# Kernel tuning notes

Measured on AMD Instinct MI355X. Metric: run time of the kernel, lower is better.

Reference implementation:

```python
import jax, jax.numpy as jnp
import numpy as np

B, L, D, O = 4, 2048, 4096, 4096   # batch, seq, in_features, out_features
P = 2                               # n_pack
NF = 2000                           # n_frequency
NFP = NF // P                       # frequencies per pack
IN_P, OUT_P = D // P, O // P        # per-pack spectrum grid
NGATE = P * D // 10                 # gate parameter count
SCALING = 150.0


def setup_inputs() -> dict:
    key = jax.random.key(0)
    ks = jax.random.split(key, 6)
    x = jax.random.normal(ks[0], (B, L, D), dtype=jnp.float32)
    base_w = jax.random.normal(ks[1], (O, D), dtype=jnp.float32) * 0.02
    base_b = jax.random.normal(ks[2], (O,), dtype=jnp.float32) * 0.02
    spectrum = jax.random.normal(ks[3], (P, NFP), dtype=jnp.float32)
    B_list = jax.random.normal(ks[4], (P, P, P), dtype=jnp.float32) * 0.5
    gate_param = jax.random.normal(ks[5], (NGATE,), dtype=jnp.float32)
    # unique random frequency locations per pack (mirrors torch.randperm)
    rng = np.random.default_rng(777)
    idx = jnp.asarray(np.stack([rng.permutation(OUT_P * IN_P)[:NFP] for _ in range(P)]), dtype=jnp.int64)
    gidx = jnp.asarray(rng.permutation(P * D)[:NGATE], dtype=jnp.int64)
    return {"x": x, "base_w": base_w, "base_b": base_b, "spectrum": spectrum,
            "B_list": B_list, "gate_param": gate_param, "idx": idx, "gidx": gidx}


def _delta_weight(spec_i, idx_i, B_i, dtype):
    # scatter sparse spectrum into (OUT_P, IN_P) grid
    dense = jnp.zeros((OUT_P, IN_P), dtype).at[idx_i // IN_P, idx_i % IN_P].set(spec_i)
    A = jnp.fft.ifft2(dense).real  # (OUT_P, IN_P)
    # kron(A, B_i) -> (O, D)
    return SCALING * (A[:, None, :, None] * B_i[None, :, None, :]).reshape(O, D)


def reference(x, base_w, base_b, spectrum, B_list, gate_param, idx, gidx):
    dt = x.dtype
    # base linear
    result = jnp.einsum('bld,od->blo', x, base_w) + base_b
    # gate matrix: scatter then ifft2
    gate_m = jnp.zeros((P, D), dt).at[gidx // D, gidx % D].set(gate_param)
    gate_m = jnp.fft.ifft2(gate_m).real  # (P, D)
    gate_w = jax.nn.softmax(jnp.einsum('bld,ed->ble', x, gate_m), axis=-1)  # (B,L,P)
    # per-pack delta weights and outputs
    deltas = jax.vmap(lambda s, i, b: _delta_weight(s, i, b, dt))(spectrum, idx, B_list)  # (P,O,D)
    outputs = jnp.einsum('bld,pod->blpo', x, deltas)  # (B,L,P,O)
    final = jnp.einsum('blpo,blp->blo', outputs, gate_w)
    return (result + final).astype(dt)
```

## Files before the change

### kernel.cpp

```cpp
#include <hip/hip_runtime.h>


#define AS1 __attribute__((address_space(1)))
#define AS3 __attribute__((address_space(3)))

using bf16x8   = __attribute__((ext_vector_type(8))) __bf16;
using f32x4    = __attribute__((ext_vector_type(4))) float;
using ushort8v = __attribute__((ext_vector_type(8))) unsigned short;
using ushort4v = __attribute__((ext_vector_type(4))) unsigned short;

__device__ __forceinline__ unsigned short f2bf(float f) {
  unsigned int u = __float_as_uint(f);
  u += 0x7FFFu + ((u >> 16) & 1u);
  return (unsigned short)(u >> 16);
}

__device__ __forceinline__ void gll16(void* lds, const void* g) {
  __builtin_amdgcn_global_load_lds((AS1 void*)(g), (AS3 void*)(lds), 16, 0, 0);
}

__global__ void k_gatem(const float* __restrict__ gp, const int* __restrict__ gidx,
                        float* __restrict__ gatem, int NG) {
  int t = blockIdx.x * 256 + threadIdx.x;
  int e = t >> 12, d = t & 4095;
  float acc = 0.f;
  for (int k = 0; k < NG; k++) {
    int iv = gidx[k];
    int dk = iv & 4095;
    float th = (float)((d * dk) & 4095) * 1.5339807878856412e-3f;
    float cv = __cosf(th);
    float v = gp[k] * cv;
    acc += ((e & (iv >> 12)) & 1) ? -v : v;
  }
  gatem[t] = acc * (1.f / 8192.f);
}

__global__ void k_tables(const float* __restrict__ spec, const int* __restrict__ idx,
                         unsigned short* __restrict__ tbl, int NFP) {
  int z = blockIdx.y;
  int p = z >> 1, isQ = z & 1;
  int t = blockIdx.x * 256 + threadIdx.x;
  int r = t >> 11, kk = t & 2047;
  unsigned short v = 0;
  if (kk < 2 * NFP) {
    int j = (kk < NFP) ? kk : kk - NFP;
    int iv = idx[p * NFP + j];
    int f = isQ ? (iv & 2047) : (iv >> 11);
    float th = (float)((r * f) & 2047) * 3.0679615757712823e-3f;
    float val = (kk < NFP) ? __cosf(th) : __sinf(th);
    if (isQ) {
      float s = spec[p * NFP + j];
      val *= (kk < NFP) ? s : -s;
    }
    v = f2bf(val);
  }
  tbl[(size_t)z * 4194304 + t] = v;
}

__global__ void k_gate(const float* __restrict__ x, const float* __restrict__ gatem,
                       float* __restrict__ g) {
  int n = blockIdx.x * 4 + (threadIdx.x >> 6);
  int l = threadIdx.x & 63;
  const float4* xr  = (const float4*)(x + (size_t)n * 4096);
  const float4* g0p = (const float4*)(gatem);
  const float4* g1p = (const float4*)(gatem + 4096);
  float s0 = 0.f, s1 = 0.f;
  for (int t = 0; t < 16; t++) {
    int ii = l + (t << 6);
    float4 xv = xr[ii], a = g0p[ii], b = g1p[ii];
    s0 += xv.x * a.x + xv.y * a.y + xv.z * a.z + xv.w * a.w;
    s1 += xv.x * b.x + xv.y * b.y + xv.z * b.z + xv.w * b.w;
  }
  for (int off = 32; off > 0; off >>= 1) {
    s0 += __shfl_down(s0, off);
    s1 += __shfl_down(s1, off);
  }
  if (l == 0) {
    float mx = fmaxf(s0, s1);
    float e0 = __expf(s0 - mx), e1 = __expf(s1 - mx);
    float inv = 1.f / (e0 + e1);
    g[2 * n] = e0 * inv;
    g[2 * n + 1] = e1 * inv;
  }
}

__global__ void k_convx(const float* __restrict__ x, unsigned short* __restrict__ xb,
                        unsigned short* __restrict__ Zg, const float* __restrict__ Bl,
                        const float* __restrict__ g) {
  size_t t = (size_t)blockIdx.x * 256 + threadIdx.x;
  const float4* xp = (const float4*)x + t * 2;
  float4 v0 = xp[0], v1 = xp[1];
  ushort8v xv;
  xv[0]=f2bf(v0.x); xv[1]=f2bf(v0.y); xv[2]=f2bf(v0.z); xv[3]=f2bf(v0.w);
  xv[4]=f2bf(v1.x); xv[5]=f2bf(v1.y); xv[6]=f2bf(v1.z); xv[7]=f2bf(v1.w);
  *(ushort8v*)(xb + t * 8) = xv;
  int n = (int)(t >> 9);
  int c0 = ((int)t & 511) * 4;
  float gg[2] = {g[2 * n], g[2 * n + 1]};
  float xe[4] = {v0.x, v0.z, v1.x, v1.z};
  float xo[4] = {v0.y, v0.w, v1.y, v1.w};
  #pragma unroll
  for (int pa = 0; pa < 4; pa++) {
    int p = pa >> 1, a = pa & 1;
    float b0 = Bl[pa * 2] * gg[p], b1 = Bl[pa * 2 + 1] * gg[p];
    ushort4v yv;
    #pragma unroll
    for (int c = 0; c < 4; c++) yv[c] = f2bf(b0 * xe[c] + b1 * xo[c]);
    *(ushort4v*)(Zg + (size_t)a * 33554432 + (size_t)n * 4096 + p * 2048 + c0) = yv;
  }
}

__global__ void k_convw(const float* __restrict__ w, unsigned short* __restrict__ wb) {
  size_t t = (size_t)blockIdx.x * 256 + threadIdx.x;
  const float4* sp = (const float4*)w + t * 2;
  float4 v0 = sp[0], v1 = sp[1];
  ushort8v o;
  o[0]=f2bf(v0.x); o[1]=f2bf(v0.y); o[2]=f2bf(v0.z); o[3]=f2bf(v0.w);
  o[4]=f2bf(v1.x); o[5]=f2bf(v1.y); o[6]=f2bf(v1.z); o[7]=f2bf(v1.w);
  *(ushort8v*)(wb + t * 8) = o;
}

__device__ __forceinline__ void gemm_core(
    const unsigned short* __restrict__ Amat, int lda,
    const unsigned short* __restrict__ Bmat, int ldb,
    int K, char* As, char* Bs, f32x4 acc[4][4]) {
  const int tid = threadIdx.x;
  const int w = tid >> 6, l = tid & 63;
  const int quad = l >> 4, l15 = l & 15;
  const int wm = (w >> 1) << 6, wn = (w & 1) << 6;

  int c1 = (w << 6) + l, c2 = c1 + 256;
  int r1 = c1 >> 2, q1 = (c1 & 3) ^ ((r1 >> 1) & 3);
  int r2 = c2 >> 2, q2 = (c2 & 3) ^ ((r2 >> 1) & 3);
  const unsigned short* aS1 = Amat + (size_t)r1 * lda + (q1 << 3);
  const unsigned short* aS2 = Amat + (size_t)r2 * lda + (q2 << 3);
  const unsigned short* bS1 = Bmat + (size_t)r1 * ldb + (q1 << 3);
  const unsigned short* bS2 = Bmat + (size_t)r2 * ldb + (q2 << 3);
  char* aD1 = As + (w << 10);
  char* aD2 = As + 4096 + (w << 10);
  char* bD1 = Bs + (w << 10);
  char* bD2 = Bs + 4096 + (w << 10);

  int aOff[4], bOff[4];
  #pragma unroll
  for (int i = 0; i < 4; i++) {
    int ra = wm + (i << 4) + l15;
    aOff[i] = (ra << 6) + ((quad ^ ((ra >> 1) & 3)) << 4);
    int rb = wn + (i << 4) + l15;
    bOff[i] = (rb << 6) + ((quad ^ ((rb >> 1) & 3)) << 4);
  }

  for (int kt = 0; kt < K; kt += 32) {
    __syncthreads();
    gll16(aD1, aS1); gll16(aD2, aS2);
    gll16(bD1, bS1); gll16(bD2, bS2);
    __syncthreads();
    bf16x8 af[4], bfv[4];
    #pragma unroll
    for (int i = 0; i < 4; i++) af[i]  = *(const bf16x8*)(As + aOff[i]);
    #pragma unroll
    for (int j = 0; j < 4; j++) bfv[j] = *(const bf16x8*)(Bs + bOff[j]);
    #pragma unroll
    for (int i = 0; i < 4; i++)
      #pragma unroll
      for (int j = 0; j < 4; j++)
        acc[i][j] = __builtin_amdgcn_mfma_f32_16x16x32_bf16(af[i], bfv[j], acc[i][j], 0, 0, 0);
    aS1 += 32; aS2 += 32; bS1 += 32; bS2 += 32;
  }
}

__global__ __launch_bounds__(256, 2) void k_abuild(
    const unsigned short* __restrict__ tbl, unsigned short* __restrict__ Acat) {
  __shared__ __align__(16) char sm[16384];
  const int p = blockIdx.z;
  const unsigned short* P = tbl + (size_t)(2 * p) * 4194304;
  const unsigned short* Q = tbl + (size_t)(2 * p + 1) * 4194304;
  f32x4 acc[4][4];
  #pragma unroll
  for (int i = 0; i < 4; i++)
    #pragma unroll
    for (int j = 0; j < 4; j++) acc[i][j] = (f32x4){0.f, 0.f, 0.f, 0.f};
  const int m0 = blockIdx.x << 7, n0 = blockIdx.y << 7;
  gemm_core(P + (size_t)m0 * 2048, 2048, Q + (size_t)n0 * 2048, 2048, 2048,
            sm, sm + 8192, acc);
  const int tid = threadIdx.x, w = tid >> 6, l = tid & 63;
  const int quad = l >> 4, l15 = l & 15;
  const int wm = (w >> 1) << 6, wn = (w & 1) << 6;
  const float SC = 150.f / 4194304.f;
  unsigned short* Ap = Acat + (size_t)p * 2048;
  #pragma unroll
  for (int j = 0; j < 4; j++) {
    int c = n0 + wn + (j << 4) + l15;
    #pragma unroll
    for (int i = 0; i < 4; i++) {
      int rb = m0 + wm + (i << 4) + (quad << 2);
      #pragma unroll
      for (int reg = 0; reg < 4; reg++)
        Ap[(size_t)(rb + reg) * 4096 + c] = f2bf(acc[i][j][reg] * SC);
    }
  }
}

__global__ __launch_bounds__(256, 2) void k_base(
    const unsigned short* __restrict__ xb, const unsigned short* __restrict__ wb,
    const float* __restrict__ bias, float* __restrict__ out) {
  __shared__ __align__(16) char sm[16384];
  f32x4 acc[4][4];
  #pragma unroll
  for (int i = 0; i < 4; i++)
    #pragma unroll
    for (int j = 0; j < 4; j++) acc[i][j] = (f32x4){0.f, 0.f, 0.f, 0.f};
  const int m0 = blockIdx.y << 7, n0 = blockIdx.x << 7;
  gemm_core(xb + (size_t)m0 * 4096, 4096, wb + (size_t)n0 * 4096, 4096, 4096,
            sm, sm + 8192, acc);
  const int tid = threadIdx.x, w = tid >> 6, l = tid & 63;
  const int quad = l >> 4, l15 = l & 15;
  const int wm = (w >> 1) << 6, wn = (w & 1) << 6;
  #pragma unroll
  for (int j = 0; j < 4; j++) {
    int o = n0 + wn + (j << 4) + l15;
    float bv = bias[o];
    #pragma unroll
    for (int i = 0; i < 4; i++) {
      int mb = m0 + wm + (i << 4) + (quad << 2);
      #pragma unroll
      for (int reg = 0; reg < 4; reg++)
        out[(size_t)(mb + reg) * 4096 + o] = acc[i][j][reg] + bv;
    }
  }
}

__global__ __launch_bounds__(256, 2) void k_pack(
    const unsigned short* __restrict__ Zg, const unsigned short* __restrict__ Acat,
    float* __restrict__ out) {
  __shared__ __align__(16) char sm[16384];
  char* Z0s = sm; char* Z1s = sm + 4096; char* Bs = sm + 8192;
  const int tid = threadIdx.x, w = tid >> 6, l = tid & 63;
  const int quad = l >> 4, l15 = l & 15;
  const int m0 = blockIdx.y << 6, r0 = blockIdx.x << 7;
  const int wm = (w >> 1) << 5, wn = (w & 1) << 6;

  int c1 = (w << 6) + l, c2 = c1 + 256;
  int rz = c1 >> 2, qz = (c1 & 3) ^ ((rz >> 1) & 3);
  int rb1 = c1 >> 2, qb1 = qz;
  int rb2 = c2 >> 2, qb2 = (c2 & 3) ^ ((rb2 >> 1) & 3);

  const unsigned short* z0S = Zg + (size_t)(m0 + rz) * 4096 + (qz << 3);
  const unsigned short* z1S = z0S + 33554432;
  const unsigned short* bS1 = Acat + (size_t)(r0 + rb1) * 4096 + (qb1 << 3);
  const unsigned short* bS2 = Acat + (size_t)(r0 + rb2) * 4096 + (qb2 << 3);
  char* z0D = Z0s + (w << 10);
  char* z1D = Z1s + (w << 10);
  char* bD1 = Bs + (w << 10);
  char* bD2 = Bs + 4096 + (w << 10);

  int zOff[2], bOff[4];
  #pragma unroll
  for (int i = 0; i < 2; i++) {
    int ra = wm + (i << 4) + l15;
    zOff[i] = (ra << 6) + ((quad ^ ((ra >> 1) & 3)) << 4);
  }
  #pragma unroll
  for (int j = 0; j < 4; j++) {
    int rb = wn + (j << 4) + l15;
    bOff[j] = (rb << 6) + ((quad ^ ((rb >> 1) & 3)) << 4);
  }

  f32x4 acc[2][2][4];
  #pragma unroll
  for (int a = 0; a < 2; a++)
    #pragma unroll
    for (int i = 0; i < 2; i++)
      #pragma unroll
      for (int j = 0; j < 4; j++) acc[a][i][j] = (f32x4){0.f, 0.f, 0.f, 0.f};

  for (int kt = 0; kt < 4096; kt += 32) {
    __syncthreads();
    gll16(z0D, z0S); gll16(z1D, z1S);
    gll16(bD1, bS1); gll16(bD2, bS2);
    __syncthreads();
    bf16x8 zf0[2], zf1[2], bfr[4];
    #pragma unroll
    for (int i = 0; i < 2; i++) {
      zf0[i] = *(const bf16x8*)(Z0s + zOff[i]);
      zf1[i] = *(const bf16x8*)(Z1s + zOff[i]);
    }
    #pragma unroll
    for (int j = 0; j < 4; j++) bfr[j] = *(const bf16x8*)(Bs + bOff[j]);
    #pragma unroll
    for (int i = 0; i < 2; i++)
      #pragma unroll
      for (int j = 0; j < 4; j++) {
        acc[0][i][j] = __builtin_amdgcn_mfma_f32_16x16x32_bf16(zf0[i], bfr[j], acc[0][i][j], 0, 0, 0);
        acc[1][i][j] = __builtin_amdgcn_mfma_f32_16x16x32_bf16(zf1[i], bfr[j], acc[1][i][j], 0, 0, 0);
      }
    z0S += 32; z1S += 32; bS1 += 32; bS2 += 32;
  }

  #pragma unroll
  for (int i = 0; i < 2; i++)
    #pragma unroll
    for (int reg = 0; reg < 4; reg++) {
      size_t n = m0 + wm + (i << 4) + (quad << 2) + reg;
      #pragma unroll
      for (int j = 0; j < 4; j++) {
        int r = r0 + wn + (j << 4) + l15;
        float2* po = (float2*)(out + n * 4096 + 2 * r);
        float2 v = *po;
        v.x += acc[0][i][j][reg];
        v.y += acc[1][i][j][reg];
        *po = v;
      }
    }
}

extern "C" void kernel_launch(void* const* d_in, const int* in_sizes, int n_in,
                              void* d_out, int out_size, void* d_ws, size_t ws_size,
                              hipStream_t stream) {
  const float* x    = (const float*)d_in[0];
  const float* basw = (const float*)d_in[1];
  const float* basb = (const float*)d_in[2];
  const float* spec = (const float*)d_in[3];
  const float* Bl   = (const float*)d_in[4];
  const float* gp   = (const float*)d_in[5];
  const int*   idx  = (const int*)d_in[6];
  const int*   gidx = (const int*)d_in[7];
  const int NFP = in_sizes[3] / 2;
  const int NG  = in_sizes[5];

  char* ws = (char*)d_ws;
  float*          gbuf  = (float*)(ws);
  float*          gatem = (float*)(ws + (64ull << 10));
  unsigned short* Acat  = (unsigned short*)(ws + (1ull << 20));
  unsigned short* xb    = (unsigned short*)(ws + (32ull << 20));
  unsigned short* bwb   = (unsigned short*)(ws + (96ull << 20));
  unsigned short* Zg    = (unsigned short*)(ws + (128ull << 20));
  unsigned short* tbl   = (unsigned short*)(ws + (128ull << 20));
  float* outp = (float*)d_out;

  k_gatem <<<32, 256, 0, stream>>>(gp, gidx, gatem, NG);
  k_tables<<<dim3(16384, 4), 256, 0, stream>>>(spec, idx, tbl, NFP);
  k_abuild<<<dim3(16, 16, 2), 256, 0, stream>>>(tbl, Acat);
  k_gate  <<<2048, 256, 0, stream>>>(x, gatem, gbuf);
  k_convx <<<16384, 256, 0, stream>>>(x, xb, Zg, Bl, gbuf);
  k_convw <<<8192, 256, 0, stream>>>(basw, bwb);
  k_base  <<<dim3(32, 64), 256, 0, stream>>>(xb, bwb, basb, outp);
  k_pack  <<<dim3(16, 128), 256, 0, stream>>>(Zg, Acat, outp);
  (void)n_in; (void)out_size; (void)ws_size;
}
```

Before: 1.117 ms.

## Use 256x256 double-buffered pipelined GEMM tiles for base and pack kernels

Replaces the 128x128 single-buffered GEMM cores of the base linear and pack kernels with a shared 256x256-tile, 512-thread routine. The new routine double-buffers LDS via global_load_lds with explicit vmcnt waits, raises wave priority around the MFMA blocks, and remaps block IDs for L2 locality. The pack kernel now handles one pack half per block instead of both interleaved, so output updates become strided scalar read-modify-writes. The goal is more data reuse per LDS load and overlap of loads with MFMA work, at the cost of 64KB LDS per block, higher register pressure and lower occupancy.

```diff
diff --git a/kernel.cpp b/kernel.cpp
--- a/kernel.cpp
+++ b/kernel.cpp
@@ -201,28 +201,110 @@
   }
 }
 
-__global__ __launch_bounds__(256, 2) void k_base(
+__device__ __forceinline__ void gemm256(const unsigned short* __restrict__ Ap,
+                                        const unsigned short* __restrict__ Bp,
+                                        char* sm, f32x4 acc[8][4]) {
+  const int tid = threadIdx.x;
+  const int wid = tid >> 6, lane = tid & 63;
+  const int quad = lane >> 4, l15 = lane & 15;
+  const int wr = wid >> 2, wc = wid & 3;
+  const int srow = tid >> 2, g = tid & 3;
+  const int q = g ^ ((srow >> 1) & 3);
+  const size_t soff = (size_t)srow * 4096 + (size_t)(q << 3);
+  const int slotx = (quad ^ ((l15 >> 1) & 3)) << 4;
+  const int aB = (((wr << 7) + l15) << 6) + slotx;
+  const int bB = (((wc << 6) + l15) << 6) + slotx + 16384;
+
+#define STG(BUF, ISB, RR, KT)                                                  \
+  gll16(sm + (BUF) * 32768 + (ISB) * 16384 + (RR) * 8192 + (wid << 10),        \
+        ((ISB) ? Bp : Ap) + soff + (size_t)(RR) * 524288 + (KT))
+
+  STG(0, 0, 0, 0);  STG(0, 0, 1, 0);
+  STG(0, 1, 0, 0);  STG(0, 1, 1, 0);
+  STG(1, 0, 0, 32); STG(1, 0, 1, 32);
+  asm volatile("s_waitcnt vmcnt(2)" ::: "memory");
+  __builtin_amdgcn_s_barrier();
+
+  bf16x8 af[8], bfv[4];
+  for (int it = 0; it < 64; it++) {
+    const int kt = it << 6;
+    const bool pref = (it < 63);
+    #pragma unroll
+    for (int i = 0; i < 8; i++) af[i]  = *(const bf16x8*)(sm + aB + i * 1024);
+    #pragma unroll
+    for (int j = 0; j < 4; j++) bfv[j] = *(const bf16x8*)(sm + bB + j * 1024);
+    STG(1, 1, 0, kt + 32); STG(1, 1, 1, kt + 32);
+    asm volatile("s_waitcnt lgkmcnt(0)" ::: "memory");
+    __builtin_amdgcn_s_setprio(1);
+    #pragma unroll
+    for (int i = 0; i < 4; i++)
+      #pragma unroll
+      for (int j = 0; j < 4; j++)
+        acc[i][j] = __builtin_amdgcn_mfma_f32_16x16x32_bf16(af[i], bfv[j], acc[i][j], 0, 0, 0);
+    __builtin_amdgcn_s_setprio(0);
+    __builtin_amdgcn_s_barrier();
+    if (pref) { STG(0, 0, 0, kt + 64); STG(0, 0, 1, kt + 64); }
+    __builtin_amdgcn_s_setprio(1);
+    #pragma unroll
+    for (int i = 4; i < 8; i++)
+      #pragma unroll
+      for (int j = 0; j < 4; j++)
+        acc[i][j] = __builtin_amdgcn_mfma_f32_16x16x32_bf16(af[i], bfv[j], acc[i][j], 0, 0, 0);
+    __builtin_amdgcn_s_setprio(0);
+    if (pref) asm volatile("s_waitcnt vmcnt(2)" ::: "memory");
+    else      asm volatile("s_waitcnt vmcnt(0)" ::: "memory");
+    __builtin_amdgcn_s_barrier();
+    #pragma unroll
+    for (int i = 0; i < 8; i++) af[i]  = *(const bf16x8*)(sm + 32768 + aB + i * 1024);
+    #pragma unroll
+    for (int j = 0; j < 4; j++) bfv[j] = *(const bf16x8*)(sm + 32768 + bB + j * 1024);
+    if (pref) { STG(0, 1, 0, kt + 64); STG(0, 1, 1, kt + 64); }
+    asm volatile("s_waitcnt lgkmcnt(0)" ::: "memory");
+    __builtin_amdgcn_s_setprio(1);
+    #pragma unroll
+    for (int i = 0; i < 4; i++)
+      #pragma unroll
+      for (int j = 0; j < 4; j++)
+        acc[i][j] = __builtin_amdgcn_mfma_f32_16x16x32_bf16(af[i], bfv[j], acc[i][j], 0, 0, 0);
+    __builtin_amdgcn_s_setprio(0);
+    __builtin_amdgcn_s_barrier();
+    if (pref) { STG(1, 0, 0, kt + 96); STG(1, 0, 1, kt + 96); }
+    __builtin_amdgcn_s_setprio(1);
+    #pragma unroll
+    for (int i = 4; i < 8; i++)
+      #pragma unroll
+      for (int j = 0; j < 4; j++)
+        acc[i][j] = __builtin_amdgcn_mfma_f32_16x16x32_bf16(af[i], bfv[j], acc[i][j], 0, 0, 0);
+    __builtin_amdgcn_s_setprio(0);
+    if (pref) asm volatile("s_waitcnt vmcnt(2)" ::: "memory");
+    __builtin_amdgcn_s_barrier();
+  }
+#undef STG
+}
+
+__global__ __launch_bounds__(512, 2) void k_base(
     const unsigned short* __restrict__ xb, const unsigned short* __restrict__ wb,
     const float* __restrict__ bias, float* __restrict__ out) {
-  __shared__ __align__(16) char sm[16384];
-  f32x4 acc[4][4];
-  #pragma unroll
-  for (int i = 0; i < 4; i++)
+  __shared__ __align__(16) char sm[65536];
+  int lid = blockIdx.x + (blockIdx.y << 4);
+  int nl = ((lid & 7) << 6) + (lid >> 3);
+  const int m0 = (nl >> 4) << 8, n0 = (nl & 15) << 8;
+  f32x4 acc[8][4];
+  #pragma unroll
+  for (int i = 0; i < 8; i++)
     #pragma unroll
     for (int j = 0; j < 4; j++) acc[i][j] = (f32x4){0.f, 0.f, 0.f, 0.f};
-  const int m0 = blockIdx.y << 7, n0 = blockIdx.x << 7;
-  gemm_core(xb + (size_t)m0 * 4096, 4096, wb + (size_t)n0 * 4096, 4096, 4096,
-            sm, sm + 8192, acc);
-  const int tid = threadIdx.x, w = tid >> 6, l = tid & 63;
-  const int quad = l >> 4, l15 = l & 15;
-  const int wm = (w >> 1) << 6, wn = (w & 1) << 6;
+  gemm256(xb + (size_t)m0 * 4096, wb + (size_t)n0 * 4096, sm, acc);
+  const int tid = threadIdx.x, wid = tid >> 6, lane = tid & 63;
+  const int quad = lane >> 4, l15 = lane & 15;
+  const int wr = wid >> 2, wc = wid & 3;
   #pragma unroll
   for (int j = 0; j < 4; j++) {
-    int o = n0 + wn + (j << 4) + l15;
+    int o = n0 + (wc << 6) + (j << 4) + l15;
     float bv = bias[o];
     #pragma unroll
-    for (int i = 0; i < 4; i++) {
-      int mb = m0 + wm + (i << 4) + (quad << 2);
+    for (int i = 0; i < 8; i++) {
+      int mb = m0 + (wr << 7) + (i << 4) + (quad << 2);
       #pragma unroll
       for (int reg = 0; reg < 4; reg++)
         out[(size_t)(mb + reg) * 4096 + o] = acc[i][j][reg] + bv;
@@ -230,88 +312,38 @@
   }
 }
 
-__global__ __launch_bounds__(256, 2) void k_pack(
+__global__ __launch_bounds__(512, 2) void k_pack(
     const unsigned short* __restrict__ Zg, const unsigned short* __restrict__ Acat,
     float* __restrict__ out) {
-  __shared__ __align__(16) char sm[16384];
-  char* Z0s = sm; char* Z1s = sm + 4096; char* Bs = sm + 8192;
-  const int tid = threadIdx.x, w = tid >> 6, l = tid & 63;
-  const int quad = l >> 4, l15 = l & 15;
-  const int m0 = blockIdx.y << 6, r0 = blockIdx.x << 7;
-  const int wm = (w >> 1) << 5, wn = (w & 1) << 6;
-
-  int c1 = (w << 6) + l, c2 = c1 + 256;
-  int rz = c1 >> 2, qz = (c1 & 3) ^ ((rz >> 1) & 3);
-  int rb1 = c1 >> 2, qb1 = qz;
-  int rb2 = c2 >> 2, qb2 = (c2 & 3) ^ ((rb2 >> 1) & 3);
-
-  const unsigned short* z0S = Zg + (size_t)(m0 + rz) * 4096 + (qz << 3);
-  const unsigned short* z1S = z0S + 33554432;
-  const unsigned short* bS1 = Acat + (size_t)(r0 + rb1) * 4096 + (qb1 << 3);
-  const unsigned short* bS2 = Acat + (size_t)(r0 + rb2) * 4096 + (qb2 << 3);
-  char* z0D = Z0s + (w << 10);
-  char* z1D = Z1s + (w << 10);
-  char* bD1 = Bs + (w << 10);
-  char* bD2 = Bs + 4096 + (w << 10);
-
-  int zOff[2], bOff[4];
-  #pragma unroll
-  for (int i = 0; i < 2; i++) {
-    int ra = wm + (i << 4) + l15;
-    zOff[i] = (ra << 6) + ((quad ^ ((ra >> 1) & 3)) << 4);
-  }
+  __shared__ __align__(16) char sm[65536];
+  int lid = blockIdx.x + (blockIdx.y << 3);
+  int nl = ((lid & 7) << 6) + (lid >> 3);
+  const int bx = nl & 7, by = nl >> 3;
+  const int a = by & 1, nt = by >> 1;
+  const int r0 = bx << 8;
+  f32x4 acc[8][4];
+  #pragma unroll
+  for (int i = 0; i < 8; i++)
+    #pragma unroll
+    for (int j = 0; j < 4; j++) acc[i][j] = (f32x4){0.f, 0.f, 0.f, 0.f};
+  gemm256(Zg + ((size_t)(a << 13) + (size_t)(nt << 8)) * 4096,
+          Acat + (size_t)r0 * 4096, sm, acc);
+  const int tid = threadIdx.x, wid = tid >> 6, lane = tid & 63;
+  const int quad = lane >> 4, l15 = lane & 15;
+  const int wr = wid >> 2, wc = wid & 3;
   #pragma unroll
   for (int j = 0; j < 4; j++) {
-    int rb = wn + (j << 4) + l15;
-    bOff[j] = (rb << 6) + ((quad ^ ((rb >> 1) & 3)) << 4);
-  }
-
-  f32x4 acc[2][2][4];
-  #pragma unroll
-  for (int a = 0; a < 2; a++)
-    #pragma unroll
-    for (int i = 0; i < 2; i++)
-      #pragma unroll
-      for (int j = 0; j < 4; j++) acc[a][i][j] = (f32x4){0.f, 0.f, 0.f, 0.f};
-
-  for (int kt = 0; kt < 4096; kt += 32) {
-    __syncthreads();
-    gll16(z0D, z0S); gll16(z1D, z1S);
-    gll16(bD1, bS1); gll16(bD2, bS2);
-    __syncthreads();
-    bf16x8 zf0[2], zf1[2], bfr[4];
-    #pragma unroll
-    for (int i = 0; i < 2; i++) {
-      zf0[i] = *(const bf16x8*)(Z0s + zOff[i]);
-      zf1[i] = *(const bf16x8*)(Z1s + zOff[i]);
-    }
-    #pragma unroll
-    for (int j = 0; j < 4; j++) bfr[j] = *(const bf16x8*)(Bs + bOff[j]);
-    #pragma unroll
-    for (int i = 0; i < 2; i++)
-      #pragma unroll
-      for (int j = 0; j < 4; j++) {
-        acc[0][i][j] = __builtin_amdgcn_mfma_f32_16x16x32_bf16(zf0[i], bfr[j], acc[0][i][j], 0, 0, 0);
-        acc[1][i][j] = __builtin_amdgcn_mfma_f32_16x16x32_bf16(zf1[i], bfr[j], acc[1][i][j], 0, 0, 0);
-      }
-    z0S += 32; z1S += 32; bS1 += 32; bS2 += 32;
-  }
-
-  #pragma unroll
-  for (int i = 0; i < 2; i++)
-    #pragma unroll
-    for (int reg = 0; reg < 4; reg++) {
-      size_t n = m0 + wm + (i << 4) + (quad << 2) + reg;
-      #pragma unroll
-      for (int j = 0; j < 4; j++) {
-        int r = r0 + wn + (j << 4) + l15;
-        float2* po = (float2*)(out + n * 4096 + 2 * r);
-        float2 v = *po;
-        v.x += acc[0][i][j][reg];
-        v.y += acc[1][i][j][reg];
-        *po = v;
+    int r = r0 + (wc << 6) + (j << 4) + l15;
+    #pragma unroll
+    for (int i = 0; i < 8; i++) {
+      int nb = (nt << 8) + (wr << 7) + (i << 4) + (quad << 2);
+      #pragma unroll
+      for (int reg = 0; reg < 4; reg++) {
+        float* p = out + (size_t)(nb + reg) * 4096 + 2 * r + a;
+        *p += acc[i][j][reg];
       }
     }
+  }
 }
 
 extern "C" void kernel_launch(void* const* d_in, const int* in_sizes, int n_in,
@@ -344,7 +376,7 @@
   k_gate  <<<2048, 256, 0, stream>>>(x, gatem, gbuf);
   k_convx <<<16384, 256, 0, stream>>>(x, xb, Zg, Bl, gbuf);
   k_convw <<<8192, 256, 0, stream>>>(basw, bwb);
-  k_base  <<<dim3(32, 64), 256, 0, stream>>>(xb, bwb, basb, outp);
-  k_pack  <<<dim3(16, 128), 256, 0, stream>>>(Zg, Acat, outp);
+  k_base  <<<dim3(16, 32), 512, 0, stream>>>(xb, bwb, basb, outp);
+  k_pack  <<<dim3(8, 64), 512, 0, stream>>>(Zg, Acat, outp);
   (void)n_in; (void)out_size; (void)ws_size;
 }
```

After: 1.004 ms. 1.11x faster.
